# Kernel optimization log

Measured on AMD Instinct MI355X. Metric: run time of the kernel, lower is better.

## Reference

```python
import jax, jax.numpy as jnp
import numpy as np
from jax import lax

EPS_BN = 1e-5
EPS_NORM = 1e-12
MEM_CHUNK = 8192


def _conv(x, w, b):
    # x: [B,C,H,W], w: [O,I,3,3], stride 2, pad 1 (torch Conv2d semantics)
    y = lax.conv_general_dilated(x, w, window_strides=(2, 2),
                                 padding=((1, 1), (1, 1)),
                                 dimension_numbers=("NCHW", "OIHW", "NCHW"))
    return y + b[None, :, None, None]


def _bn(x, gamma, beta, mean, var):
    # eval-mode BatchNorm2d with running statistics
    inv = lax.rsqrt(var + EPS_BN)
    return (x - mean[None, :, None, None]) * (gamma * inv)[None, :, None, None] + beta[None, :, None, None]


def setup_inputs() -> dict:
    key = jax.random.key(0)
    ks = jax.random.split(key, 20)
    B, H = 256, 64
    N_MEM, D = 262144, 64
    inp = {
        "x": jax.random.normal(ks[0], (B, 1, H, H), dtype=jnp.float32),
        "memory_bank": jax.random.normal(ks[1], (N_MEM, D), dtype=jnp.float32),
    }
    specs = [(1, 16), (16, 32), (32, 64)]
    for i, (cin, cout) in enumerate(specs):
        fan_in = cin * 9
        bound = 1.0 / np.sqrt(fan_in)
        inp[f"w{i}"] = jax.random.uniform(ks[2 + 6 * i], (cout, cin, 3, 3), jnp.float32, -bound, bound)
        inp[f"b{i}"] = jax.random.uniform(ks[3 + 6 * i], (cout,), jnp.float32, -bound, bound)
        inp[f"gamma{i}"] = jnp.ones((cout,), jnp.float32)
        inp[f"beta{i}"] = jnp.zeros((cout,), jnp.float32)
        inp[f"mean{i}"] = 0.1 * jax.random.normal(ks[4 + 6 * i], (cout,), jnp.float32)
        inp[f"var{i}"] = jax.random.uniform(ks[5 + 6 * i], (cout,), jnp.float32, 0.5, 1.5)
    return inp


def _forward(x, memory_bank,
             w0, b0, gamma0, beta0, mean0, var0,
             w1, b1, gamma1, beta1, mean1, var1,
             w2, b2, gamma2, beta2, mean2, var2):
    B = x.shape[0]
    D = 64
    # backbone: (conv -> bn -> relu) x3, stride 2 each -> H/8
    h = x
    params = [(w0, b0, gamma0, beta0, mean0, var0),
              (w1, b1, gamma1, beta1, mean1, var1),
              (w2, b2, gamma2, beta2, mean2, var2)]
    for (w, b, g, bt, m, v) in params:
        h = jax.nn.relu(_bn(_conv(h, w, b), g, bt, m, v))
    # [B,64,8,8] -> [B,P,64], L2 normalize
    emb = h.transpose(0, 2, 3, 1).reshape(B, -1, D)
    emb = emb / jnp.clip(jnp.linalg.norm(emb, axis=-1, keepdims=True), EPS_NORM)
    P = emb.shape[1]
    q = emb.reshape(-1, D)                      # [Q, D]
    q_sq = jnp.sum(q * q, axis=-1)              # [Q]
    # memory bank is L2-normalized at set_memory_bank time
    mb = memory_bank / jnp.clip(jnp.linalg.norm(memory_bank, axis=-1, keepdims=True), EPS_NORM)
    n_chunks = mb.shape[0] // MEM_CHUNK
    mb_chunks = mb.reshape(n_chunks, MEM_CHUNK, D)

    def body(best, mc):
        # blockwise squared L2 via gram trick, online running min (never full matrix)
        d2 = q_sq[:, None] + jnp.sum(mc * mc, axis=-1)[None, :] - 2.0 * (q @ mc.T)
        d = jnp.sqrt(jnp.clip(d2, 0.0))
        return jnp.minimum(best, jnp.min(d, axis=1)), None

    best, _ = lax.scan(body, jnp.full((q.shape[0],), jnp.inf, q.dtype), mb_chunks)
    patch_dist = best.reshape(B, P)
    return jnp.max(patch_dist, axis=1)          # reduction='max'


def reference(x, memory_bank,
              w0, b0, gamma0, beta0, mean0, var0,
              w1, b1, gamma1, beta1, mean1, var1,
              w2, b2, gamma2, beta2, mean2, var2):
    return _forward(x, memory_bank,
                    w0, b0, gamma0, beta0, mean0, var0,
                    w1, b1, gamma1, beta1, mean1, var1,
                    w2, b2, gamma2, beta2, mean2, var2)
```

## Files before the change

kernel.cpp:

```cpp
#include <hip/hip_runtime.h>
#include <math.h>

typedef __bf16 v8bf __attribute__((ext_vector_type(8)));
typedef __bf16 v4bf __attribute__((ext_vector_type(4)));
typedef float  v16f __attribute__((ext_vector_type(16)));
typedef float  v4f  __attribute__((ext_vector_type(4)));

#define EPS_BN 1e-5f
#define Q_TOTAL 16384
#define N_MEM   262144
#define SLICES  64
#define SLICE_LEN (N_MEM / SLICES)
#define CHUNK   128
#define NCHUNKS (SLICE_LEN / CHUNK)

__device__ __forceinline__ void gload_lds16(const void* g, void* l) {
    __builtin_amdgcn_global_load_lds(
        (const __attribute__((address_space(1))) void*)g,
        (__attribute__((address_space(3))) void*)l, 16, 0, 0);
}

__global__ void conv0_kernel(const float* __restrict__ x,
                             const float* __restrict__ w, const float* __restrict__ bias,
                             const float* __restrict__ gamma, const float* __restrict__ beta,
                             const float* __restrict__ mean, const float* __restrict__ var,
                             float* __restrict__ out) {
    int idx = blockIdx.x * 256 + threadIdx.x;
    int xo = idx & 31, yo = (idx >> 5) & 31, c = (idx >> 10) & 15, b = idx >> 14;
    const float* xp = x + (size_t)b * 4096;
    const float* wc = w + c * 9;
    float acc = 0.f;
#pragma unroll
    for (int dy = 0; dy < 3; ++dy) {
        int iy = 2 * yo + dy - 1;
        if (iy < 0) continue;
#pragma unroll
        for (int dx = 0; dx < 3; ++dx) {
            int ix = 2 * xo + dx - 1;
            if (ix < 0) continue;
            acc += wc[dy * 3 + dx] * xp[iy * 64 + ix];
        }
    }
    acc += bias[c];
    float sc = gamma[c] * rsqrtf(var[c] + EPS_BN);
    float v  = (acc - mean[c]) * sc + beta[c];
    out[idx] = fmaxf(v, 0.f);
}

__global__ void conv1_kernel(const float* __restrict__ in,
                             const float* __restrict__ w, const float* __restrict__ bias,
                             const float* __restrict__ gamma, const float* __restrict__ beta,
                             const float* __restrict__ mean, const float* __restrict__ var,
                             float* __restrict__ out) {
    __shared__ float in_s[16384];
    __shared__ float sc_s[8], sh_s[8];
    int b = blockIdx.x >> 2, cg = blockIdx.x & 3;
    int t = threadIdx.x;
    const float4* ip4 = (const float4*)(in + (size_t)b * 16384);
    float4* is4 = (float4*)in_s;
    for (int i = t; i < 4096; i += 256) is4[i] = ip4[i];
    if (t < 8) {
        int c = cg * 8 + t;
        float sc = gamma[c] * rsqrtf(var[c] + EPS_BN);
        sc_s[t] = sc;
        sh_s[t] = (bias[c] - mean[c]) * sc + beta[c];
    }
    __syncthreads();
    const float* wg = w + cg * 1152;
    int xo = t & 15, yo = t >> 4;
    float acc[8];
#pragma unroll
    for (int c = 0; c < 8; ++c) acc[c] = 0.f;
    int iy0 = 2 * yo - 1, ix0 = 2 * xo - 1;
    for (int ci = 0; ci < 16; ++ci) {
        const float* base = in_s + ci * 1024;
        float r[9];
#pragma unroll
        for (int dy = 0; dy < 3; ++dy) {
            int iy = iy0 + dy;
            int iyc = iy < 0 ? 0 : iy;
#pragma unroll
            for (int dx = 0; dx < 3; ++dx) {
                int ix = ix0 + dx;
                int ixc = ix < 0 ? 0 : ix;
                float v = base[iyc * 32 + ixc];
                r[dy * 3 + dx] = (iy >= 0 && ix >= 0) ? v : 0.f;
            }
        }
#pragma unroll
        for (int c = 0; c < 8; ++c) {
            const float* wp = wg + (c * 16 + ci) * 9;
#pragma unroll
            for (int k = 0; k < 9; ++k) acc[c] = fmaf(wp[k], r[k], acc[c]);
        }
    }
#pragma unroll
    for (int c = 0; c < 8; ++c) {
        float v = fmaf(acc[c], sc_s[c], sh_s[c]);
        out[((size_t)(b * 32 + cg * 8 + c) * 16 + yo) * 16 + xo] = fmaxf(v, 0.f);
    }
}

__global__ void conv2_kernel(const float* __restrict__ in,
                             const float* __restrict__ w, const float* __restrict__ bias,
                             const float* __restrict__ gamma, const float* __restrict__ beta,
                             const float* __restrict__ mean, const float* __restrict__ var,
                             float* __restrict__ out) {
    __shared__ float in_s[8192];
    __shared__ float sc_s[16], sh_s[16];
    int b = blockIdx.x >> 2, cg = blockIdx.x & 3;
    int t = threadIdx.x;
    const float4* ip4 = (const float4*)(in + (size_t)b * 8192);
    float4* is4 = (float4*)in_s;
    for (int i = t; i < 2048; i += 256) is4[i] = ip4[i];
    if (t < 16) {
        int c = cg * 16 + t;
        float sc = gamma[c] * rsqrtf(var[c] + EPS_BN);
        sc_s[t] = sc;
        sh_s[t] = (bias[c] - mean[c]) * sc + beta[c];
    }
    __syncthreads();
    const float* wg = w + cg * 4608;
    int xo = t & 7, yo = (t >> 3) & 7, cs = t >> 6;
    float acc[4];
#pragma unroll
    for (int l = 0; l < 4; ++l) acc[l] = 0.f;
    int iy0 = 2 * yo - 1, ix0 = 2 * xo - 1;
    for (int ci = 0; ci < 32; ++ci) {
        const float* base = in_s + ci * 256;
        float r[9];
#pragma unroll
        for (int dy = 0; dy < 3; ++dy) {
            int iy = iy0 + dy;
            int iyc = iy < 0 ? 0 : iy;
#pragma unroll
            for (int dx = 0; dx < 3; ++dx) {
                int ix = ix0 + dx;
                int ixc = ix < 0 ? 0 : ix;
                float v = base[iyc * 16 + ixc];
                r[dy * 3 + dx] = (iy >= 0 && ix >= 0) ? v : 0.f;
            }
        }
#pragma unroll
        for (int l = 0; l < 4; ++l) {
            const float* wp = wg + ((cs * 4 + l) * 32 + ci) * 9;
#pragma unroll
            for (int k = 0; k < 9; ++k) acc[l] = fmaf(wp[k], r[k], acc[l]);
        }
    }
#pragma unroll
    for (int l = 0; l < 4; ++l) {
        int c = cg * 16 + cs * 4 + l;
        float v = fmaf(acc[l], sc_s[cs * 4 + l], sh_s[cs * 4 + l]);
        out[((size_t)(b * 64 + c) * 8 + yo) * 8 + xo] = fmaxf(v, 0.f);
    }
}

__global__ void qnorm_kernel(const float* __restrict__ y2,
                             __bf16* __restrict__ q, float* __restrict__ qsq,
                             unsigned int* __restrict__ mind2) {
    int b = blockIdx.x, t = threadIdx.x;
    if (t < 64) mind2[b * 64 + t] = 0x7f800000u;
    int p = t >> 2, dg = t & 3;
    const float* src = y2 + (size_t)b * 4096 + p;
    float v[16];
    float ss = 0.f;
#pragma unroll
    for (int i = 0; i < 16; ++i) {
        v[i] = src[(dg * 16 + i) * 64];
        ss += v[i] * v[i];
    }
    ss += __shfl_xor(ss, 1, 64);
    ss += __shfl_xor(ss, 2, 64);
    float inv = 1.f / fmaxf(sqrtf(ss), 1e-12f);
    v8bf o0, o1;
    float q2 = 0.f;
#pragma unroll
    for (int i = 0; i < 16; ++i) {
        __bf16 bv = (__bf16)(v[i] * inv);
        if (i < 8) o0[i] = bv; else o1[i - 8] = bv;
        float fb = (float)bv;
        q2 += fb * fb;
    }
    q2 += __shfl_xor(q2, 1, 64);
    q2 += __shfl_xor(q2, 2, 64);
    if (dg == 0) qsq[b * 64 + p] = q2;
    __bf16* dst = q + ((size_t)(b * 64 + p)) * 64 + dg * 16;
    *(v8bf*)dst = o0;
    *(v8bf*)(dst + 8) = o1;
}

__global__ void mbnorm_kernel(const float* __restrict__ mb,
                              __bf16* __restrict__ mbbf) {
    int tid = blockIdx.x * 256 + threadIdx.x;
    int row = tid >> 4, sub = tid & 15;
    const float4 v = *(const float4*)(mb + (size_t)row * 64 + sub * 4);
    float ss = v.x * v.x + v.y * v.y + v.z * v.z + v.w * v.w;
#pragma unroll
    for (int o = 1; o < 16; o <<= 1) ss += __shfl_xor(ss, o, 64);
    float inv = 1.f / fmaxf(sqrtf(ss), 1e-12f);
    v4bf o;
    o[0] = (__bf16)(v.x * inv);
    o[1] = (__bf16)(v.y * inv);
    o[2] = (__bf16)(v.z * inv);
    o[3] = (__bf16)(v.w * inv);
    *(v4bf*)(mbbf + (size_t)row * 64 + sub * 4) = o;
}

__global__ __launch_bounds__(256, 4)
void dist_kernel(const __bf16* __restrict__ q, const float* __restrict__ qsq,
                 const __bf16* __restrict__ mb,
                 unsigned int* __restrict__ mind2) {
    __shared__ __align__(16) __bf16 Bs[2][CHUNK * 64];
    const int t = threadIdx.x;
    const int wave = t >> 6, lane = t & 63;
    const int c16 = lane & 15;
    const int kblk = lane >> 4;
    const int mbase = blockIdx.x * 256 + wave * 64;
    const int slice = blockIdx.y;

    v8bf a[4][2];
#pragma unroll
    for (int s = 0; s < 4; ++s)
#pragma unroll
        for (int ks = 0; ks < 2; ++ks)
            a[s][ks] = *(const v8bf*)(q + (size_t)(mbase + s * 16 + c16) * 64
                                        + ks * 32 + kblk * 8);

    float tmax[4][4];
#pragma unroll
    for (int s = 0; s < 4; ++s)
#pragma unroll
        for (int r = 0; r < 4; ++r) tmax[s][r] = -3.0e38f;

    v4f Z;
#pragma unroll
    for (int r = 0; r < 4; ++r) Z[r] = 0.f;

    const int r0 = t >> 3, c0 = (t & 7) ^ (r0 & 7);
    const __bf16* gp = mb + (size_t)slice * SLICE_LEN * 64 + r0 * 64 + c0 * 8;
    const int wbase = wave * 1024;

#pragma unroll
    for (int j = 0; j < 4; ++j) {
        gload_lds16(gp, (char*)Bs[0] + j * 4096 + wbase);
        gp += 2048;
    }

    const int rowb = c16 * 128;
    int offk[2];
#pragma unroll
    for (int ks = 0; ks < 2; ++ks) offk[ks] = (((kblk + 4 * ks) ^ (lane & 7)) << 4);

    auto step = [&](const char* bp, char* pdst, bool more) {
        __syncthreads();
        if (more) {
#pragma unroll
            for (int j = 0; j < 4; ++j) {
                gload_lds16(gp, pdst + j * 4096 + wbase);
                gp += 2048;
            }
        }
        const char* tp = bp + rowb;
        v8bf be[2], bo[2];
#pragma unroll
        for (int ks = 0; ks < 2; ++ks) {
            be[ks] = *(const v8bf*)(tp + offk[ks]);
            bo[ks] = *(const v8bf*)(tp + 2048 + offk[ks]);
        }
#pragma unroll 1
        for (int p = 0; p < 4; ++p) {
            v4f Ae[4], Ao[4];
#pragma unroll
            for (int s = 0; s < 4; ++s)
                Ae[s] = __builtin_amdgcn_mfma_f32_16x16x32_bf16(a[s][0], be[0], Z, 0, 0, 0);
#pragma unroll
            for (int s = 0; s < 4; ++s)
                Ao[s] = __builtin_amdgcn_mfma_f32_16x16x32_bf16(a[s][0], bo[0], Z, 0, 0, 0);
#pragma unroll
            for (int s = 0; s < 4; ++s)
                Ae[s] = __builtin_amdgcn_mfma_f32_16x16x32_bf16(a[s][1], be[1], Ae[s], 0, 0, 0);
#pragma unroll
            for (int s = 0; s < 4; ++s)
                Ao[s] = __builtin_amdgcn_mfma_f32_16x16x32_bf16(a[s][1], bo[1], Ao[s], 0, 0, 0);
            if (p < 3) {
                const char* tn = tp + (p + 1) * 4096;
#pragma unroll
                for (int ks = 0; ks < 2; ++ks) {
                    be[ks] = *(const v8bf*)(tn + offk[ks]);
                    bo[ks] = *(const v8bf*)(tn + 2048 + offk[ks]);
                }
            }
#pragma unroll
            for (int s = 0; s < 4; ++s)
#pragma unroll
                for (int r = 0; r < 4; ++r)
                    tmax[s][r] = fmaxf(fmaxf(Ae[s][r], Ao[s][r]), tmax[s][r]);
        }
    };

    for (int ch = 0; ch < NCHUNKS; ch += 2) {
        step((const char*)Bs[0], (char*)Bs[1], ch + 1 < NCHUNKS);
        step((const char*)Bs[1], (char*)Bs[0], ch + 2 < NCHUNKS);
    }

#pragma unroll
    for (int s = 0; s < 4; ++s)
#pragma unroll
        for (int r = 0; r < 4; ++r) {
            float v = tmax[s][r];
            v = fmaxf(v, __shfl_xor(v, 1, 64));
            v = fmaxf(v, __shfl_xor(v, 2, 64));
            v = fmaxf(v, __shfl_xor(v, 4, 64));
            v = fmaxf(v, __shfl_xor(v, 8, 64));
            tmax[s][r] = v;
        }
    if (c16 == 0) {
#pragma unroll
        for (int s = 0; s < 4; ++s)
#pragma unroll
            for (int r = 0; r < 4; ++r) {
                int m = mbase + s * 16 + kblk * 4 + r;
                float dd = fmaxf(qsq[m] + 1.0f - 2.0f * tmax[s][r], 0.f);
                atomicMin(mind2 + m, __float_as_uint(dd));
            }
    }
}

__global__ void finalize_kernel(const unsigned int* __restrict__ mind2,
                                float* __restrict__ out) {
    int b = blockIdx.x, l = threadIdx.x;
    float v = __uint_as_float(mind2[b * 64 + l]);
    float d = sqrtf(fmaxf(v, 0.f));
#pragma unroll
    for (int o = 1; o < 64; o <<= 1) d = fmaxf(d, __shfl_xor(d, o, 64));
    if (l == 0) out[b] = d;
}

extern "C" void kernel_launch(void* const* d_in, const int* in_sizes, int n_in,
                              void* d_out, int out_size, void* d_ws, size_t ws_size,
                              hipStream_t stream) {
    (void)in_sizes; (void)n_in; (void)out_size; (void)ws_size;
    const float* x     = (const float*)d_in[0];
    const float* mbank = (const float*)d_in[1];
    const float* w0 = (const float*)d_in[2],  *b0 = (const float*)d_in[3];
    const float* g0 = (const float*)d_in[4],  *be0 = (const float*)d_in[5];
    const float* mn0 = (const float*)d_in[6], *vr0 = (const float*)d_in[7];
    const float* w1 = (const float*)d_in[8],  *b1 = (const float*)d_in[9];
    const float* g1 = (const float*)d_in[10], *be1 = (const float*)d_in[11];
    const float* mn1 = (const float*)d_in[12], *vr1 = (const float*)d_in[13];
    const float* w2 = (const float*)d_in[14], *b2 = (const float*)d_in[15];
    const float* g2 = (const float*)d_in[16], *be2 = (const float*)d_in[17];
    const float* mn2 = (const float*)d_in[18], *vr2 = (const float*)d_in[19];

    char* ws = (char*)d_ws;
    float*        y0    = (float*)(ws + 0);
    float*        y1    = (float*)(ws + 16777216);
    float*        y2    = (float*)(ws + 25165824);
    __bf16*       qbf   = (__bf16*)(ws + 29360128);
    float*        qsq   = (float*)(ws + 31457280);
    __bf16*       mbbf  = (__bf16*)(ws + 31522816);
    unsigned int* mind2 = (unsigned int*)(ws + 66125824);

    conv0_kernel<<<16384, 256, 0, stream>>>(x, w0, b0, g0, be0, mn0, vr0, y0);
    conv1_kernel<<<1024, 256, 0, stream>>>(y0, w1, b1, g1, be1, mn1, vr1, y1);
    conv2_kernel<<<1024, 256, 0, stream>>>(y1, w2, b2, g2, be2, mn2, vr2, y2);
    qnorm_kernel<<<256, 256, 0, stream>>>(y2, qbf, qsq, mind2);
    mbnorm_kernel<<<16384, 256, 0, stream>>>(mbank, mbbf);
    dist_kernel<<<dim3(64, SLICES), 256, 0, stream>>>(qbf, qsq, mbbf, mind2);
    finalize_kernel<<<256, 64, 0, stream>>>(mind2, (float*)d_out);
}
```

Before: 558.4 us.

## Fuse conv2 with query normalization and load each image's input once

Conv1 and conv2 now run one 512-thread block per image covering all output channels, instead of four blocks per image that each reloaded the same input into LDS. Conv2 is fused with the query L2-normalize/bf16-pack step by staging outputs in a padded LDS tile, which removes the y2 round trip through global memory and one kernel launch. In exchange the grids shrink to 256 blocks each, which lowers parallelism, and each thread keeps more accumulators in registers.

```diff
diff --git a/kernel.cpp b/kernel.cpp
--- a/kernel.cpp
+++ b/kernel.cpp
@@ -53,24 +53,23 @@
                              const float* __restrict__ mean, const float* __restrict__ var,
                              float* __restrict__ out) {
     __shared__ float in_s[16384];
-    __shared__ float sc_s[8], sh_s[8];
-    int b = blockIdx.x >> 2, cg = blockIdx.x & 3;
-    int t = threadIdx.x;
+    __shared__ float sc_s[32], sh_s[32];
+    int b = blockIdx.x, t = threadIdx.x;
     const float4* ip4 = (const float4*)(in + (size_t)b * 16384);
     float4* is4 = (float4*)in_s;
-    for (int i = t; i < 4096; i += 256) is4[i] = ip4[i];
-    if (t < 8) {
-        int c = cg * 8 + t;
-        float sc = gamma[c] * rsqrtf(var[c] + EPS_BN);
+    for (int i = t; i < 4096; i += 512) is4[i] = ip4[i];
+    if (t < 32) {
+        float sc = gamma[t] * rsqrtf(var[t] + EPS_BN);
         sc_s[t] = sc;
-        sh_s[t] = (bias[c] - mean[c]) * sc + beta[c];
+        sh_s[t] = (bias[t] - mean[t]) * sc + beta[t];
     }
     __syncthreads();
-    const float* wg = w + cg * 1152;
-    int xo = t & 15, yo = t >> 4;
-    float acc[8];
-#pragma unroll
-    for (int c = 0; c < 8; ++c) acc[c] = 0.f;
+    int px = t & 255, half = t >> 8;
+    int xo = px & 15, yo = px >> 4;
+    const float* wg = w + half * 2304;
+    float acc[16];
+#pragma unroll
+    for (int c = 0; c < 16; ++c) acc[c] = 0.f;
     int iy0 = 2 * yo - 1, ix0 = 2 * xo - 1;
     for (int ci = 0; ci < 16; ++ci) {
         const float* base = in_s + ci * 1024;
@@ -88,43 +87,46 @@
             }
         }
 #pragma unroll
-        for (int c = 0; c < 8; ++c) {
+        for (int c = 0; c < 16; ++c) {
             const float* wp = wg + (c * 16 + ci) * 9;
 #pragma unroll
             for (int k = 0; k < 9; ++k) acc[c] = fmaf(wp[k], r[k], acc[c]);
         }
     }
 #pragma unroll
-    for (int c = 0; c < 8; ++c) {
-        float v = fmaf(acc[c], sc_s[c], sh_s[c]);
-        out[((size_t)(b * 32 + cg * 8 + c) * 16 + yo) * 16 + xo] = fmaxf(v, 0.f);
-    }
-}
-
-__global__ void conv2_kernel(const float* __restrict__ in,
-                             const float* __restrict__ w, const float* __restrict__ bias,
-                             const float* __restrict__ gamma, const float* __restrict__ beta,
-                             const float* __restrict__ mean, const float* __restrict__ var,
-                             float* __restrict__ out) {
+    for (int c = 0; c < 16; ++c) {
+        int ch = half * 16 + c;
+        float v = fmaf(acc[c], sc_s[ch], sh_s[ch]);
+        out[((size_t)(b * 32 + ch) * 16 + yo) * 16 + xo] = fmaxf(v, 0.f);
+    }
+}
+
+__global__ void conv2q_kernel(const float* __restrict__ in,
+                              const float* __restrict__ w, const float* __restrict__ bias,
+                              const float* __restrict__ gamma, const float* __restrict__ beta,
+                              const float* __restrict__ mean, const float* __restrict__ var,
+                              __bf16* __restrict__ q, float* __restrict__ qsq,
+                              unsigned int* __restrict__ mind2) {
     __shared__ float in_s[8192];
-    __shared__ float sc_s[16], sh_s[16];
-    int b = blockIdx.x >> 2, cg = blockIdx.x & 3;
-    int t = threadIdx.x;
+    __shared__ float out_s[64 * 65];
+    __shared__ float sc_s[64], sh_s[64];
+    int b = blockIdx.x, t = threadIdx.x;
+    if (t < 64) mind2[b * 64 + t] = 0x7f800000u;
     const float4* ip4 = (const float4*)(in + (size_t)b * 8192);
     float4* is4 = (float4*)in_s;
-    for (int i = t; i < 2048; i += 256) is4[i] = ip4[i];
-    if (t < 16) {
-        int c = cg * 16 + t;
-        float sc = gamma[c] * rsqrtf(var[c] + EPS_BN);
+    for (int i = t; i < 2048; i += 512) is4[i] = ip4[i];
+    if (t < 64) {
+        float sc = gamma[t] * rsqrtf(var[t] + EPS_BN);
         sc_s[t] = sc;
-        sh_s[t] = (bias[c] - mean[c]) * sc + beta[c];
+        sh_s[t] = (bias[t] - mean[t]) * sc + beta[t];
     }
     __syncthreads();
-    const float* wg = w + cg * 4608;
-    int xo = t & 7, yo = (t >> 3) & 7, cs = t >> 6;
-    float acc[4];
-#pragma unroll
-    for (int l = 0; l < 4; ++l) acc[l] = 0.f;
+    int px = t & 63, oct = t >> 6;
+    int xo = px & 7, yo = px >> 3;
+    const float* wg = w + oct * 2304;
+    float acc[8];
+#pragma unroll
+    for (int c = 0; c < 8; ++c) acc[c] = 0.f;
     int iy0 = 2 * yo - 1, ix0 = 2 * xo - 1;
     for (int ci = 0; ci < 32; ++ci) {
         const float* base = in_s + ci * 256;
@@ -142,52 +144,45 @@
             }
         }
 #pragma unroll
-        for (int l = 0; l < 4; ++l) {
-            const float* wp = wg + ((cs * 4 + l) * 32 + ci) * 9;
-#pragma unroll
-            for (int k = 0; k < 9; ++k) acc[l] = fmaf(wp[k], r[k], acc[l]);
-        }
-    }
-#pragma unroll
-    for (int l = 0; l < 4; ++l) {
-        int c = cg * 16 + cs * 4 + l;
-        float v = fmaf(acc[l], sc_s[cs * 4 + l], sh_s[cs * 4 + l]);
-        out[((size_t)(b * 64 + c) * 8 + yo) * 8 + xo] = fmaxf(v, 0.f);
-    }
-}
-
-__global__ void qnorm_kernel(const float* __restrict__ y2,
-                             __bf16* __restrict__ q, float* __restrict__ qsq,
-                             unsigned int* __restrict__ mind2) {
-    int b = blockIdx.x, t = threadIdx.x;
-    if (t < 64) mind2[b * 64 + t] = 0x7f800000u;
-    int p = t >> 2, dg = t & 3;
-    const float* src = y2 + (size_t)b * 4096 + p;
-    float v[16];
+        for (int c = 0; c < 8; ++c) {
+            const float* wp = wg + (c * 32 + ci) * 9;
+#pragma unroll
+            for (int k = 0; k < 9; ++k) acc[c] = fmaf(wp[k], r[k], acc[c]);
+        }
+    }
+#pragma unroll
+    for (int c = 0; c < 8; ++c) {
+        int ch = oct * 8 + c;
+        float v = fmaf(acc[c], sc_s[ch], sh_s[ch]);
+        out_s[px * 65 + ch] = fmaxf(v, 0.f);
+    }
+    __syncthreads();
+    int p2 = t >> 3, dg = t & 7;
+    float vv[8];
     float ss = 0.f;
 #pragma unroll
-    for (int i = 0; i < 16; ++i) {
-        v[i] = src[(dg * 16 + i) * 64];
-        ss += v[i] * v[i];
+    for (int i = 0; i < 8; ++i) {
+        vv[i] = out_s[p2 * 65 + dg * 8 + i];
+        ss += vv[i] * vv[i];
     }
     ss += __shfl_xor(ss, 1, 64);
     ss += __shfl_xor(ss, 2, 64);
+    ss += __shfl_xor(ss, 4, 64);
     float inv = 1.f / fmaxf(sqrtf(ss), 1e-12f);
-    v8bf o0, o1;
+    v8bf o;
     float q2 = 0.f;
 #pragma unroll
-    for (int i = 0; i < 16; ++i) {
-        __bf16 bv = (__bf16)(v[i] * inv);
-        if (i < 8) o0[i] = bv; else o1[i - 8] = bv;
+    for (int i = 0; i < 8; ++i) {
+        __bf16 bv = (__bf16)(vv[i] * inv);
+        o[i] = bv;
         float fb = (float)bv;
         q2 += fb * fb;
     }
     q2 += __shfl_xor(q2, 1, 64);
     q2 += __shfl_xor(q2, 2, 64);
-    if (dg == 0) qsq[b * 64 + p] = q2;
-    __bf16* dst = q + ((size_t)(b * 64 + p)) * 64 + dg * 16;
-    *(v8bf*)dst = o0;
-    *(v8bf*)(dst + 8) = o1;
+    q2 += __shfl_xor(q2, 4, 64);
+    if (dg == 0) qsq[b * 64 + p2] = q2;
+    *(v8bf*)(q + ((size_t)(b * 64 + p2)) * 64 + dg * 8) = o;
 }
 
 __global__ void mbnorm_kernel(const float* __restrict__ mb,
@@ -356,16 +351,15 @@
     char* ws = (char*)d_ws;
     float*        y0    = (float*)(ws + 0);
     float*        y1    = (float*)(ws + 16777216);
-    float*        y2    = (float*)(ws + 25165824);
     __bf16*       qbf   = (__bf16*)(ws + 29360128);
     float*        qsq   = (float*)(ws + 31457280);
     __bf16*       mbbf  = (__bf16*)(ws + 31522816);
     unsigned int* mind2 = (unsigned int*)(ws + 66125824);
 
     conv0_kernel<<<16384, 256, 0, stream>>>(x, w0, b0, g0, be0, mn0, vr0, y0);
-    conv1_kernel<<<1024, 256, 0, stream>>>(y0, w1, b1, g1, be1, mn1, vr1, y1);
-    conv2_kernel<<<1024, 256, 0, stream>>>(y1, w2, b2, g2, be2, mn2, vr2, y2);
-    qnorm_kernel<<<256, 256, 0, stream>>>(y2, qbf, qsq, mind2);
+    conv1_kernel<<<256, 512, 0, stream>>>(y0, w1, b1, g1, be1, mn1, vr1, y1);
+    conv2q_kernel<<<256, 512, 0, stream>>>(y1, w2, b2, g2, be2, mn2, vr2,
+                                           qbf, qsq, mind2);
     mbnorm_kernel<<<16384, 256, 0, stream>>>(mbank, mbbf);
     dist_kernel<<<dim3(64, SLICES), 256, 0, stream>>>(qbf, qsq, mbbf, mind2);
     finalize_kernel<<<256, 64, 0, stream>>>(mind2, (float*)d_out);
```

New measurement: 571.4 us. 1.02x slower.
